# Optimization experiments

Hardware: AMD Instinct MI355X
Metric: run time of the kernel (lower is better)

## Reference

```python
import jax, jax.numpy as jnp
import numpy as np

PATCH = 24  # self.current_patch
STRIDE = PATCH // 2


def _conv(x, w, b):
    # NCHW conv, SAME padding, stride 1 (= Conv2d(k=3, padding=1))
    y = jax.lax.conv_general_dilated(x, w, (1, 1), 'SAME',
                                     dimension_numbers=('NCHW', 'OIHW', 'NCHW'))
    return y + b[None, :, None, None]


def setup_inputs() -> dict:
    key = jax.random.key(0)
    ks = jax.random.split(key, 9)
    b, c, h, w = 2, 64, 192, 192
    s = 0.05  # keep sigmoid/tanh unsaturated
    return {
        'source': jax.random.normal(ks[0], (b, c, h, w), jnp.float32),
        'target': jax.random.normal(ks[1], (b, c, h, w), jnp.float32),
        # deform_net params (128->512->256->1)
        'W1': jax.random.normal(ks[2], (512, 128, 3, 3), jnp.float32) * s,
        'b1': jnp.zeros((512,), jnp.float32),
        'W2': jax.random.normal(ks[3], (256, 512, 3, 3), jnp.float32) * s,
        'b2': jnp.zeros((256,), jnp.float32),
        'W3': jax.random.normal(ks[4], (1, 256, 3, 3), jnp.float32) * s,
        'b3': jnp.zeros((1,), jnp.float32),
        # reg_net params (128->512->64->1); original declared 256 in-ch (bug), fixed to 128
        'Wr1': jax.random.normal(ks[5], (512, 128, 3, 3), jnp.float32) * s,
        'br1': jnp.zeros((512,), jnp.float32),
        'Wr2': jax.random.normal(ks[6], (64, 512, 3, 3), jnp.float32) * s,
        'br2': jnp.zeros((64,), jnp.float32),
        'Wr3': jax.random.normal(ks[7], (1, 64, 3, 3), jnp.float32) * s,
        'br3': jnp.zeros((1,), jnp.float32),
    }


def _attention(src, tgt, W1, b1, W2, b2, W3, b3):
    b, c, h, w = src.shape
    p, st = PATCH, STRIDE
    nH = (h - p) // st + 1
    nW = (w - p) // st + 1
    # patch gather indices
    r_idx = jnp.arange(nH)[:, None] * st + jnp.arange(p)[None, :]  # [nH, p]
    c_idx = jnp.arange(nW)[:, None] * st + jnp.arange(p)[None, :]  # [nW, p]
    # [b, c, nH, nW, p, p]
    def gather(x):
        return x[:, :, r_idx[:, None, :, None], c_idx[None, :, None, :]]
    ps = gather(src)
    pt = gather(tgt)
    # -> [b*nH*nW, 2c, p, p]  (one big batched conv replaces the python loop)
    pair = jnp.concatenate([ps, pt], axis=1)            # [b, 2c, nH, nW, p, p]
    pair = pair.transpose(0, 2, 3, 1, 4, 5).reshape(b * nH * nW, 2 * c, p, p)
    x = jax.nn.relu(_conv(pair, W1, b1))
    x = jax.nn.relu(_conv(x, W2, b2))
    score = jax.nn.sigmoid(_conv(x, W3, b3))            # [b*nH*nW, 1, p, p]
    score = score.reshape(b, nH, nW, 1, p, p).transpose(0, 3, 1, 2, 4, 5)  # [b,1,nH,nW,p,p]
    # overlap-add scatter (duplicate indices accumulate)
    R = jnp.broadcast_to(r_idx[:, None, :, None], (nH, nW, p, p))
    C = jnp.broadcast_to(c_idx[None, :, None, :], (nH, nW, p, p))
    att = jnp.zeros((b, 1, h, w), src.dtype).at[:, :, R, C].add(score)
    cnt = jnp.zeros((b, 1, h, w), src.dtype).at[:, :, R, C].add(1.0)
    return att / jnp.maximum(cnt, 1.0)


def reference(source, target, W1, b1, W2, b2, W3, b3, Wr1, br1, Wr2, br2, Wr3, br3):
    attention_map = _attention(source, target, W1, b1, W2, b2, W3, b3)
    x = jnp.concatenate([source, target], axis=1)       # [b, 128, h, w]
    x = jax.nn.relu(_conv(x, Wr1, br1))
    x = jax.nn.relu(_conv(x, Wr2, br2))
    registered = jnp.tanh(_conv(x, Wr3, br3))           # [b, 1, h, w]
    return registered, attention_map
```

## Files before the change

kernel.cpp:

```cpp
#include <hip/hip_runtime.h>
#include <cmath>

typedef _Float16 half8  __attribute__((ext_vector_type(8)));
typedef _Float16 half4v __attribute__((ext_vector_type(4)));
typedef float    float4v __attribute__((ext_vector_type(4)));

template<int N> __device__ __forceinline__ void vwait() {
    asm volatile("s_waitcnt vmcnt(%0)" :: "n"(N) : "memory");
}

template<int MT, int NT, int MODE>
__global__ __launch_bounds__(256, 2)
void mfma_conv(const _Float16* __restrict__ in, const _Float16* __restrict__ Wg,
               const float* __restrict__ bias, _Float16* __restrict__ out,
               int CI, int CO, int RSin, int RSout, int NB, int NC, int p0)
{
    constexpr int CHUNKS_PH = 3 * MT * 64;
    constexpr int STAGE_N   = CHUNKS_PH / 256;
    constexpr int VF        = STAGE_N + 9;
    __shared__ __align__(16) _Float16 sW[3][CHUNKS_PH * 8];

    const int tid  = threadIdx.x;
    const int wave = tid >> 6;
    const int lane = tid & 63;
    const int ll   = lane & 15;
    const int quad = lane >> 4;

    const int NSUB = NC * (9 / NT);
    const int id   = blockIdx.x;
    const int xcd  = id & 7;
    const int slot = id >> 3;
    const int unit = (slot / NSUB) * 8 + xcd;
    const int rem  = slot % NSUB;
    const int pxb  = rem / NC;
    const int co_t = rem % NC;
    if (unit >= NB) return;
    const int co0 = co_t * (MT * 16);
    const int pbase = pxb * (NT * 64) + wave * (NT * 16);

    if (slot & 1) __builtin_amdgcn_s_sleep(32);

    size_t in_base, out_base;
    int TY = 0, TX = 0;
    int b_off[NT], edge[NT];
    if (MODE == 0) {
        int pat = p0 + unit;
        int bb = pat / 225, remp = pat % 225;
        int pi = remp / 15, pj = remp % 15;
        in_base  = (size_t)bb * RSin * RSin * CI;
        out_base = (size_t)unit * 676 * CO;
        #pragma unroll
        for (int nt = 0; nt < NT; ++nt) {
            int p = pbase + nt * 16 + ll;
            int py = p / 24, px = p % 24;
            b_off[nt] = ((pi * 12 + py) * RSin + (pj * 12 + px)) * CI;
            edge[nt] = (py == 0 ? 1 : 0) | (py == 23 ? 2 : 0)
                     | (px == 0 ? 4 : 0) | (px == 23 ? 8 : 0);
        }
    } else if (MODE == 1) {
        in_base  = (size_t)unit * 676 * CI;
        out_base = (size_t)unit * 676 * CO;
        #pragma unroll
        for (int nt = 0; nt < NT; ++nt) {
            int p = pbase + nt * 16 + ll;
            b_off[nt] = ((p / 24) * RSin + (p % 24)) * CI;
            edge[nt] = 0;
        }
    } else {
        int tile = unit & 63, b = unit >> 6;
        TY = (tile >> 3) * 24; TX = (tile & 7) * 24;
        in_base  = (size_t)b * RSin * RSin * CI;
        out_base = (size_t)b * RSout * RSout * CO;
        #pragma unroll
        for (int nt = 0; nt < NT; ++nt) {
            int p = pbase + nt * 16 + ll;
            b_off[nt] = ((TY + p / 24) * RSin + (TX + p % 24)) * CI;
            edge[nt] = 0;
        }
    }

    auto stage = [&](int bufI, int ci0, int dy) {
        #pragma unroll
        for (int k = 0; k < STAGE_N; ++k) {
            int c = tid + k * 256;
            int lane_s = c & 63;
            int mtt = c >> 6;
            int mt = mtt % MT, dxl = mtt / MT;
            const _Float16* src =
                &Wg[((size_t)(co0 + mt * 16 + (lane_s & 15)) * 9 + (dy * 3 + dxl)) * CI
                    + ci0 + (lane_s >> 4) * 8];
            __builtin_amdgcn_global_load_lds(
                (const __attribute__((address_space(1))) void*)src,
                (__attribute__((address_space(3))) void*)&sW[bufI][(size_t)c * 8],
                16, 0, 0);
        }
    };

    auto bload = [&](uint4 (&B)[NT][3], int ci0, int dy) {
        const _Float16* inp = in + in_base + ci0 + quad * 8;
        const int rowoff = dy * RSin * CI;
        #pragma unroll
        for (int nt = 0; nt < NT; ++nt)
            #pragma unroll
            for (int dx = 0; dx < 3; ++dx)
                B[nt][dx] = *(const uint4*)(inp + b_off[nt] + rowoff + dx * CI);
    };

    float4v acc[MT][NT];
    #pragma unroll
    for (int mt = 0; mt < MT; ++mt)
        #pragma unroll
        for (int nt = 0; nt < NT; ++nt)
            acc[mt][nt] = (float4v){0.f, 0.f, 0.f, 0.f};

    auto compute = [&](int bufI, uint4 (&B)[NT][3], int dy) {
        #pragma unroll
        for (int dx = 0; dx < 3; ++dx) {
            const int emask = (dy == 0 ? 1 : 0) | (dy == 2 ? 2 : 0)
                            | (dx == 0 ? 4 : 0) | (dx == 2 ? 8 : 0);
            half8 a[MT];
            #pragma unroll
            for (int mt = 0; mt < MT; ++mt)
                a[mt] = *(const half8*)&sW[bufI][((dx * MT + mt) * 64 + lane) * 8];
            #pragma unroll
            for (int nt = 0; nt < NT; ++nt) {
                uint4 raw = B[nt][dx];
                if (MODE == 0) {
                    bool z = (edge[nt] & emask) != 0;
                    raw.x = z ? 0u : raw.x;
                    raw.y = z ? 0u : raw.y;
                    raw.z = z ? 0u : raw.z;
                    raw.w = z ? 0u : raw.w;
                }
                half8 b = *(half8*)&raw;
                #pragma unroll
                for (int mt = 0; mt < MT; ++mt)
                    acc[mt][nt] = __builtin_amdgcn_mfma_f32_16x16x32_f16(
                        a[mt], b, acc[mt][nt], 0, 0, 0);
            }
        }
    };

    uint4 bA[NT][3], bB[NT][3];

    const int phases = (CI >> 5) * 3;
    stage(0, 0, 0);
    stage(1, 0, 1);
    bload(bA, 0, 0);

    int bufC = 0, dyC = 0, ciC = 0;
    int bufS = 2, dyS = 2, ciS = 0;
    int dyB = 1, ciB = 0;

#define ADV(dy, ci) do { if (dy == 2) { dy = 0; ci += 32; } else ++dy; } while (0)
#define PH(BCUR, BNXT, HASS, HASB, VN)                                      \
    do {                                                                    \
        __builtin_amdgcn_s_barrier();                                       \
        if (HASS) { stage(bufS, ciS, dyS);                                  \
                    bufS = (bufS == 2) ? 0 : bufS + 1; ADV(dyS, ciS); }     \
        if (HASB) { bload(BNXT, ciB, dyB); ADV(dyB, ciB); }                 \
        vwait<VN>();                                                        \
        __builtin_amdgcn_sched_barrier(0);                                  \
        __builtin_amdgcn_s_setprio(1);                                      \
        compute(bufC, BCUR, dyC);                                           \
        __builtin_amdgcn_s_setprio(0);                                      \
        bufC = (bufC == 2) ? 0 : bufC + 1; ADV(dyC, ciC);                   \
    } while (0)

    for (int it = 0; it < (phases - 6) / 2; ++it) {
        PH(bA, bB, 1, 1, VF);
        PH(bB, bA, 1, 1, VF);
    }
    PH(bA, bB, 1, 1, VF);
    PH(bB, bA, 1, 1, VF);
    PH(bA, bB, 1, 1, VF);
    PH(bB, bA, 1, 1, VF);
    PH(bA, bB, 0, 1, 9);
    PH(bB, bA, 0, 0, 0);
#undef PH
#undef ADV

    #pragma unroll
    for (int mt = 0; mt < MT; ++mt) {
        float4v bs = *(const float4v*)&bias[co0 + mt * 16 + quad * 4];
        #pragma unroll
        for (int nt = 0; nt < NT; ++nt) {
            int p = pbase + nt * 16 + ll;
            size_t ooff = out_base
                + (size_t)((TY + p / 24 + 1) * RSout + (TX + p % 24) + 1) * CO
                + co0 + mt * 16 + quad * 4;
            float4v v = acc[mt][nt];
            half4v h;
            h.x = (_Float16)fmaxf(v.x + bs.x, 0.f);
            h.y = (_Float16)fmaxf(v.y + bs.y, 0.f);
            h.z = (_Float16)fmaxf(v.z + bs.z, 0.f);
            h.w = (_Float16)fmaxf(v.w + bs.w, 0.f);
            *(half4v*)(out + ooff) = h;
        }
    }
}

static inline int swiz_grid(int NB, int NC, int PXB) {
    return ((NB + 7) & ~7) * NC * PXB;
}

template<int MODE, int ACT, int NT>
__global__ __launch_bounds__(256, 2)
void mfma_score(const _Float16* __restrict__ in, const _Float16* __restrict__ W16,
                const float* __restrict__ bias, float* __restrict__ outp,
                int CI, int RSI, int NB, int PXB)
{
    __shared__ __align__(16) _Float16 sW[9 * 16 * 32];

    const int tid  = threadIdx.x;
    const int wave = tid >> 6;
    const int lane = tid & 63;
    const int ll   = lane & 15;
    const int quad = lane >> 4;

    const int unit = blockIdx.x / PXB;
    const int pxb  = blockIdx.x % PXB;
    if (unit >= NB) return;
    const int pbase = pxb * (NT * 64) + wave * (NT * 16);

    size_t in_base;
    int ty = 0, tx = 0, bb = 0;
    if (MODE == 2) {
        bb = unit >> 6; int tile = unit & 63; ty = (tile >> 3) * 24; tx = (tile & 7) * 24;
        in_base = (size_t)bb * RSI * RSI * CI;
    } else {
        in_base = (size_t)unit * 676 * CI;
    }

    int b_off[NT];
    #pragma unroll
    for (int nt = 0; nt < NT; ++nt) {
        int p = pbase + nt * 16 + ll;
        b_off[nt] = ((ty + p / 24) * RSI + (tx + p % 24)) * CI;
    }

    float4v acc[NT];
    #pragma unroll
    for (int nt = 0; nt < NT; ++nt) acc[nt] = (float4v){0.f, 0.f, 0.f, 0.f};

    for (int ci0 = 0; ci0 < CI; ci0 += 32) {
        __syncthreads();
        for (int c = tid; c < 9 * 16 * 4; c += 256) {
            int q = c & 3, tco = c >> 2;
            int t = tco >> 4, co = tco & 15;
            *(uint4*)&sW[tco * 32 + q * 8] =
                *(const uint4*)&W16[((size_t)co * 9 + t) * CI + ci0 + q * 8];
        }
        __syncthreads();

        const _Float16* inp = in + in_base + ci0 + quad * 8;
        for (int dy = 0; dy < 3; ++dy)
            for (int dx = 0; dx < 3; ++dx) {
                const int t = dy * 3 + dx;
                const int toff = (dy * RSI + dx) * CI;
                half8 a = *(const half8*)&sW[(t * 16 + ll) * 32 + quad * 8];
                #pragma unroll
                for (int nt = 0; nt < NT; ++nt) {
                    half8 b = *(const half8*)(inp + b_off[nt] + toff);
                    acc[nt] = __builtin_amdgcn_mfma_f32_16x16x32_f16(a, b, acc[nt], 0, 0, 0);
                }
            }
    }

    if (quad == 0) {
        float bv = bias[0];
        #pragma unroll
        for (int nt = 0; nt < NT; ++nt) {
            int p = pbase + nt * 16 + ll;
            float v = acc[nt].x + bv;
            if (ACT == 1) {
                outp[(size_t)unit * 576 + p] = 1.f / (1.f + expf(-v));
            } else {
                int y = ty + p / 24, x = tx + p % 24;
                outp[(size_t)bb * 36864 + y * 192 + x] = tanhf(v);
            }
        }
    }
}

__global__ __launch_bounds__(256)
void build_x16i(const float* __restrict__ src, const float* __restrict__ tgt,
                _Float16* __restrict__ X)
{
    int idx = blockIdx.x * 256 + threadIdx.x;
    int q = idx & 15, pid = idx >> 4;
    if (pid >= 2 * 36864) return;
    int b = pid / 36864, r = pid % 36864;
    int y = r / 192, x = r % 192;
    half8 h;
    #pragma unroll
    for (int j = 0; j < 8; ++j) {
        int ch = q * 8 + j;
        const float* im = (ch < 64) ? src : tgt;
        h[j] = (_Float16)im[(size_t)(b * 64 + (ch & 63)) * 36864 + r];
    }
    *(half8*)&X[(((size_t)b * 194 + y + 1) * 194 + (x + 1)) * 128 + q * 8] = h;
}

__global__ __launch_bounds__(256)
void cvt_w(const float* __restrict__ src, _Float16* __restrict__ dst, int CO, int CI)
{
    int idx = blockIdx.x * 256 + threadIdx.x;
    if (idx >= CO * 9 * CI) return;
    int ci = idx % CI, t = (idx / CI) % 9, co = idx / (9 * CI);
    dst[idx] = (_Float16)src[((size_t)co * CI + ci) * 9 + t];
}

__global__ __launch_bounds__(256)
void cvt_pad16(const float* __restrict__ src, _Float16* __restrict__ dst, int CI)
{
    int idx = blockIdx.x * 256 + threadIdx.x;
    if (idx >= 16 * 9 * CI) return;
    int ci = idx % CI, t = (idx / CI) % 9, co = idx / (9 * CI);
    dst[idx] = (co == 0) ? (_Float16)src[(size_t)ci * 9 + t] : (_Float16)0.0f;
}

__global__ __launch_bounds__(256)
void ring_zero(_Float16* __restrict__ buf, int npatch, int RS, int CI)
{
    int c8 = CI >> 3;
    int RC = 2 * RS + 2 * (RS - 2);
    int idx = blockIdx.x * 256 + threadIdx.x;
    if (idx >= npatch * RC * c8) return;
    int q = idx % c8, rp = (idx / c8) % RC, pl = idx / (c8 * RC);
    int r, c;
    if (rp < RS)            { r = 0;      c = rp; }
    else if (rp < 2 * RS)   { r = RS - 1; c = rp - RS; }
    else {
        int s = rp - 2 * RS, half = RS - 2;
        if (s < half) { r = s + 1;        c = 0; }
        else          { r = s - half + 1; c = RS - 1; }
    }
    uint4 z = {0u, 0u, 0u, 0u};
    *(uint4*)&buf[((size_t)pl * RS * RS + r * RS + c) * CI + q * 8] = z;
}

__global__ __launch_bounds__(256)
void att_finalize(const float* __restrict__ score, float* __restrict__ out)
{
    int idx = blockIdx.x * 256 + threadIdx.x;
    if (idx >= 2 * 36864) return;
    int b = idx / 36864, r = idx % 36864;
    int y = r / 192, x = r % 192;
    int i_lo = (y >= 24) ? (y - 12) / 12 : 0;
    int i_hi = min(14, y / 12);
    int j_lo = (x >= 24) ? (x - 12) / 12 : 0;
    int j_hi = min(14, x / 12);
    float s = 0.f; int cnt = 0;
    for (int i = i_lo; i <= i_hi; ++i)
        for (int j = j_lo; j <= j_hi; ++j) {
            s += score[(((size_t)b * 15 + i) * 15 + j) * 576 + (y - 12 * i) * 24 + (x - 12 * j)];
            ++cnt;
        }
    out[idx] = s / (float)cnt;
}

extern "C" void kernel_launch(void* const* d_in, const int* in_sizes, int n_in,
                              void* d_out, int out_size, void* d_ws, size_t ws_size,
                              hipStream_t stream)
{
    const float* src = (const float*)d_in[0];
    const float* tgt = (const float*)d_in[1];
    const float* W1  = (const float*)d_in[2];  const float* b1  = (const float*)d_in[3];
    const float* W2  = (const float*)d_in[4];  const float* b2  = (const float*)d_in[5];
    const float* W3  = (const float*)d_in[6];  const float* b3  = (const float*)d_in[7];
    const float* Wr1 = (const float*)d_in[8];  const float* br1 = (const float*)d_in[9];
    const float* Wr2 = (const float*)d_in[10]; const float* br2 = (const float*)d_in[11];
    const float* Wr3 = (const float*)d_in[12]; const float* br3 = (const float*)d_in[13];
    float* out = (float*)d_out;

    _Float16* ws = (_Float16*)d_ws;
    size_t o = 0;
    _Float16* X16i = ws + o; o += (size_t)2 * 194 * 194 * 128;
    _Float16* W1h  = ws + o; o += (size_t)512 * 9 * 128;
    _Float16* W2h  = ws + o; o += (size_t)256 * 9 * 512;
    _Float16* Wr1h = ws + o; o += (size_t)512 * 9 * 128;
    _Float16* Wr2h = ws + o; o += (size_t)64 * 9 * 512;
    _Float16* W3p  = ws + o; o += (size_t)16 * 9 * 256;
    _Float16* Wr3p = ws + o; o += (size_t)16 * 9 * 64;
    float*    score = (float*)(ws + o); o += 2 * 259200;
    const size_t fixed_h = o;

    const size_t per_patch_h = (size_t)676 * (512 + 256);
    const size_t regA_h = (size_t)2 * 194 * 194 * 512;
    const size_t regB_h = (size_t)2 * 194 * 194 * 64;
    size_t h_avail = ws_size / 2;
    int P = 50;
    {
        size_t n450 = 450 * per_patch_h; if (n450 < regA_h + regB_h) n450 = regA_h + regB_h;
        size_t n150 = 150 * per_patch_h; if (n150 < regA_h + regB_h) n150 = regA_h + regB_h;
        if (h_avail >= fixed_h + n450)      P = 450;
        else if (h_avail >= fixed_h + n150) P = 150;
    }
    const int nchunks = 450 / P;

    _Float16* D1 = ws + fixed_h;
    _Float16* D2 = D1 + (size_t)P * 676 * 512;

    ring_zero<<<(2 * 772 * 16 + 255) / 256, 256, 0, stream>>>(X16i, 2, 194, 128);
    build_x16i<<<4608, 256, 0, stream>>>(src, tgt, X16i);
    cvt_w<<<2304, 256, 0, stream>>>(W1,  W1h,  512, 128);
    cvt_w<<<4608, 256, 0, stream>>>(W2,  W2h,  256, 512);
    cvt_w<<<2304, 256, 0, stream>>>(Wr1, Wr1h, 512, 128);
    cvt_w<<<1152, 256, 0, stream>>>(Wr2, Wr2h, 64,  512);
    cvt_pad16<<<(16 * 9 * 256 + 255) / 256, 256, 0, stream>>>(W3,  W3p,  256);
    cvt_pad16<<<(16 * 9 * 64  + 255) / 256, 256, 0, stream>>>(Wr3, Wr3p, 64);

    ring_zero<<<(P * 100 * 64 + 255) / 256, 256, 0, stream>>>(D1, P, 26, 512);
    ring_zero<<<(P * 100 * 32 + 255) / 256, 256, 0, stream>>>(D2, P, 26, 256);
    for (int c = 0; c < nchunks; ++c) {
        int p0 = c * P;
        mfma_conv<8, 3, 0><<<swiz_grid(P, 4, 3), 256, 0, stream>>>(
            X16i, W1h, b1, D1, 128, 512, 194, 26, P, 4, p0);
        mfma_conv<8, 3, 1><<<swiz_grid(P, 2, 3), 256, 0, stream>>>(
            D1, W2h, b2, D2, 512, 256, 26, 26, P, 2, 0);
        mfma_score<1, 1, 3><<<P * 3, 256, 0, stream>>>(
            D2, W3p, b3, score + (size_t)p0 * 576, 256, 26, P, 3);
    }
    att_finalize<<<288, 256, 0, stream>>>(score, out + 73728);

    {
        _Float16* A1 = ws + fixed_h;
        _Float16* A2 = A1 + ((P >= 150) ? regA_h : (size_t)194 * 194 * 512);
        if (P >= 150) {
            ring_zero<<<(2 * 772 * 64 + 255) / 256, 256, 0, stream>>>(A1, 2, 194, 512);
            ring_zero<<<(2 * 772 * 8  + 255) / 256, 256, 0, stream>>>(A2, 2, 194, 64);
            mfma_conv<8, 3, 2><<<swiz_grid(128, 4, 3), 256, 0, stream>>>(
                X16i, Wr1h, br1, A1, 128, 512, 194, 194, 128, 4, 0);
            mfma_conv<4, 3, 2><<<swiz_grid(128, 1, 3), 256, 0, stream>>>(
                A1, Wr2h, br2, A2, 512, 64, 194, 194, 128, 1, 0);
            mfma_score<2, 2, 3><<<128 * 3, 256, 0, stream>>>(
                A2, Wr3p, br3, out, 64, 194, 128, 3);
        } else {
            for (int b = 0; b < 2; ++b) {
                ring_zero<<<(772 * 64 + 255) / 256, 256, 0, stream>>>(A1, 1, 194, 512);
                ring_zero<<<(772 * 8  + 255) / 256, 256, 0, stream>>>(A2, 1, 194, 64);
                mfma_conv<8, 3, 2><<<swiz_grid(64, 4, 3), 256, 0, stream>>>(
                    X16i + (size_t)b * 194 * 194 * 128, Wr1h, br1, A1,
                    128, 512, 194, 194, 64, 4, 0);
                mfma_conv<4, 3, 2><<<swiz_grid(64, 1, 3), 256, 0, stream>>>(
                    A1, Wr2h, br2, A2, 512, 64, 194, 194, 64, 1, 0);
                mfma_score<2, 2, 3><<<64 * 3, 256, 0, stream>>>(
                    A2, Wr3p, br3, out + (size_t)b * 36864, 64, 194, 64, 3);
            }
        }
    }
}
```

Before: 2.231 ms.

## Flatten pixel tiling across patches and retile conv to MT=4, NT=4

```diff
diff --git a/kernel.cpp b/kernel.cpp
--- a/kernel.cpp
+++ b/kernel.cpp
@@ -17,7 +17,9 @@
 {
     constexpr int CHUNKS_PH = 3 * MT * 64;
     constexpr int STAGE_N   = CHUNKS_PH / 256;
-    constexpr int VF        = STAGE_N + 9;
+    constexpr int BLOAD_N   = 3 * NT;
+    constexpr int VF        = STAGE_N + BLOAD_N;
+    constexpr int PXBLK     = NT * 64;
     __shared__ __align__(16) _Float16 sW[3][CHUNKS_PH * 8];
 
     const int tid  = threadIdx.x;
@@ -26,55 +28,52 @@
     const int ll   = lane & 15;
     const int quad = lane >> 4;
 
-    const int NSUB = NC * (9 / NT);
+    const int Gpx  = (NB * 576 + PXBLK - 1) / PXBLK;
     const int id   = blockIdx.x;
     const int xcd  = id & 7;
     const int slot = id >> 3;
-    const int unit = (slot / NSUB) * 8 + xcd;
-    const int rem  = slot % NSUB;
-    const int pxb  = rem / NC;
-    const int co_t = rem % NC;
-    if (unit >= NB) return;
+    const int pxblk = (slot / NC) * 8 + xcd;
+    const int co_t  = slot % NC;
+    if (pxblk >= Gpx) return;
     const int co0 = co_t * (MT * 16);
-    const int pbase = pxb * (NT * 64) + wave * (NT * 16);
-
-    if (slot & 1) __builtin_amdgcn_s_sleep(32);
-
-    size_t in_base, out_base;
-    int TY = 0, TX = 0;
-    int b_off[NT], edge[NT];
-    if (MODE == 0) {
-        int pat = p0 + unit;
-        int bb = pat / 225, remp = pat % 225;
-        int pi = remp / 15, pj = remp % 15;
-        in_base  = (size_t)bb * RSin * RSin * CI;
-        out_base = (size_t)unit * 676 * CO;
-        #pragma unroll
-        for (int nt = 0; nt < NT; ++nt) {
-            int p = pbase + nt * 16 + ll;
-            int py = p / 24, px = p % 24;
-            b_off[nt] = ((pi * 12 + py) * RSin + (pj * 12 + px)) * CI;
+    const int pg0 = pxblk * PXBLK + wave * (NT * 16);
+
+    size_t b_off[NT], obase[NT];
+    int edge[NT];
+    bool valid[NT];
+    #pragma unroll
+    for (int nt = 0; nt < NT; ++nt) {
+        int pgn = pg0 + nt * 16 + ll;
+        int u = pgn / 576;
+        int p = pgn - u * 576;
+        valid[nt] = (u < NB);
+        int uu = valid[nt] ? u : 0;
+        int py = p / 24, px = p % 24;
+        if (MODE == 0) {
+            int pat = p0 + uu;
+            int bb = pat / 225, remp = pat % 225;
+            int pi = remp / 15, pj = remp % 15;
+            b_off[nt] = (size_t)bb * RSin * RSin * CI
+                      + (size_t)((pi * 12 + py) * RSin + (pj * 12 + px)) * CI
+                      + quad * 8;
+            obase[nt] = (size_t)uu * 676 * CO
+                      + (size_t)((py + 1) * RSout + (px + 1)) * CO;
             edge[nt] = (py == 0 ? 1 : 0) | (py == 23 ? 2 : 0)
                      | (px == 0 ? 4 : 0) | (px == 23 ? 8 : 0);
-        }
-    } else if (MODE == 1) {
-        in_base  = (size_t)unit * 676 * CI;
-        out_base = (size_t)unit * 676 * CO;
-        #pragma unroll
-        for (int nt = 0; nt < NT; ++nt) {
-            int p = pbase + nt * 16 + ll;
-            b_off[nt] = ((p / 24) * RSin + (p % 24)) * CI;
+        } else if (MODE == 1) {
+            b_off[nt] = (size_t)uu * 676 * CI + (size_t)(py * RSin + px) * CI
+                      + quad * 8;
+            obase[nt] = (size_t)uu * 676 * CO
+                      + (size_t)((py + 1) * RSout + (px + 1)) * CO;
             edge[nt] = 0;
-        }
-    } else {
-        int tile = unit & 63, b = unit >> 6;
-        TY = (tile >> 3) * 24; TX = (tile & 7) * 24;
-        in_base  = (size_t)b * RSin * RSin * CI;
-        out_base = (size_t)b * RSout * RSout * CO;
-        #pragma unroll
-        for (int nt = 0; nt < NT; ++nt) {
-            int p = pbase + nt * 16 + ll;
-            b_off[nt] = ((TY + p / 24) * RSin + (TX + p % 24)) * CI;
+        } else {
+            int bb = uu >> 6, tile = uu & 63;
+            int TY = (tile >> 3) * 24, TX = (tile & 7) * 24;
+            b_off[nt] = (size_t)bb * RSin * RSin * CI
+                      + (size_t)((TY + py) * RSin + (TX + px)) * CI
+                      + quad * 8;
+            obase[nt] = (size_t)bb * RSout * RSout * CO
+                      + (size_t)((TY + py + 1) * RSout + (TX + px + 1)) * CO;
             edge[nt] = 0;
         }
     }
@@ -97,13 +96,12 @@
     };
 
     auto bload = [&](uint4 (&B)[NT][3], int ci0, int dy) {
-        const _Float16* inp = in + in_base + ci0 + quad * 8;
-        const int rowoff = dy * RSin * CI;
+        const size_t rowoff = (size_t)(dy * RSin) * CI + ci0;
         #pragma unroll
         for (int nt = 0; nt < NT; ++nt)
             #pragma unroll
             for (int dx = 0; dx < 3; ++dx)
-                B[nt][dx] = *(const uint4*)(inp + b_off[nt] + rowoff + dx * CI);
+                B[nt][dx] = *(const uint4*)(in + b_off[nt] + rowoff + dx * CI);
     };
 
     float4v acc[MT][NT];
@@ -167,15 +165,11 @@
         bufC = (bufC == 2) ? 0 : bufC + 1; ADV(dyC, ciC);                   \
     } while (0)
 
-    for (int it = 0; it < (phases - 6) / 2; ++it) {
+    for (int it = 0; it < (phases - 2) / 2; ++it) {
         PH(bA, bB, 1, 1, VF);
         PH(bB, bA, 1, 1, VF);
     }
-    PH(bA, bB, 1, 1, VF);
-    PH(bB, bA, 1, 1, VF);
-    PH(bA, bB, 1, 1, VF);
-    PH(bB, bA, 1, 1, VF);
-    PH(bA, bB, 0, 1, 9);
+    PH(bA, bB, 0, 1, BLOAD_N);
     PH(bB, bA, 0, 0, 0);
 #undef PH
 #undef ADV
@@ -185,10 +179,8 @@
         float4v bs = *(const float4v*)&bias[co0 + mt * 16 + quad * 4];
         #pragma unroll
         for (int nt = 0; nt < NT; ++nt) {
-            int p = pbase + nt * 16 + ll;
-            size_t ooff = out_base
-                + (size_t)((TY + p / 24 + 1) * RSout + (TX + p % 24) + 1) * CO
-                + co0 + mt * 16 + quad * 4;
+            if (!valid[nt]) continue;
+            size_t ooff = obase[nt] + co0 + mt * 16 + quad * 4;
             float4v v = acc[mt][nt];
             half4v h;
             h.x = (_Float16)fmaxf(v.x + bs.x, 0.f);
@@ -200,8 +192,9 @@
     }
 }
 
-static inline int swiz_grid(int NB, int NC, int PXB) {
-    return ((NB + 7) & ~7) * NC * PXB;
+static inline int swiz_gridpx(int NB, int NT, int NC) {
+    int Gpx = (NB * 576 + NT * 64 - 1) / (NT * 64);
+    return ((Gpx + 7) & ~7) * NC;
 }
 
 template<int MODE, int ACT, int NT>
@@ -415,10 +408,10 @@
     ring_zero<<<(P * 100 * 32 + 255) / 256, 256, 0, stream>>>(D2, P, 26, 256);
     for (int c = 0; c < nchunks; ++c) {
         int p0 = c * P;
-        mfma_conv<8, 3, 0><<<swiz_grid(P, 4, 3), 256, 0, stream>>>(
-            X16i, W1h, b1, D1, 128, 512, 194, 26, P, 4, p0);
-        mfma_conv<8, 3, 1><<<swiz_grid(P, 2, 3), 256, 0, stream>>>(
-            D1, W2h, b2, D2, 512, 256, 26, 26, P, 2, 0);
+        mfma_conv<4, 4, 0><<<swiz_gridpx(P, 4, 8), 256, 0, stream>>>(
+            X16i, W1h, b1, D1, 128, 512, 194, 26, P, 8, p0);
+        mfma_conv<4, 4, 1><<<swiz_gridpx(P, 4, 4), 256, 0, stream>>>(
+            D1, W2h, b2, D2, 512, 256, 26, 26, P, 4, 0);
         mfma_score<1, 1, 3><<<P * 3, 256, 0, stream>>>(
             D2, W3p, b3, score + (size_t)p0 * 576, 256, 26, P, 3);
     }
@@ -430,9 +423,9 @@
         if (P >= 150) {
             ring_zero<<<(2 * 772 * 64 + 255) / 256, 256, 0, stream>>>(A1, 2, 194, 512);
             ring_zero<<<(2 * 772 * 8  + 255) / 256, 256, 0, stream>>>(A2, 2, 194, 64);
-            mfma_conv<8, 3, 2><<<swiz_grid(128, 4, 3), 256, 0, stream>>>(
-                X16i, Wr1h, br1, A1, 128, 512, 194, 194, 128, 4, 0);
-            mfma_conv<4, 3, 2><<<swiz_grid(128, 1, 3), 256, 0, stream>>>(
+            mfma_conv<4, 4, 2><<<swiz_gridpx(128, 4, 8), 256, 0, stream>>>(
+                X16i, Wr1h, br1, A1, 128, 512, 194, 194, 128, 8, 0);
+            mfma_conv<4, 4, 2><<<swiz_gridpx(128, 4, 1), 256, 0, stream>>>(
                 A1, Wr2h, br2, A2, 512, 64, 194, 194, 128, 1, 0);
             mfma_score<2, 2, 3><<<128 * 3, 256, 0, stream>>>(
                 A2, Wr3p, br3, out, 64, 194, 128, 3);
@@ -440,10 +433,10 @@
             for (int b = 0; b < 2; ++b) {
                 ring_zero<<<(772 * 64 + 255) / 256, 256, 0, stream>>>(A1, 1, 194, 512);
                 ring_zero<<<(772 * 8  + 255) / 256, 256, 0, stream>>>(A2, 1, 194, 64);
-                mfma_conv<8, 3, 2><<<swiz_grid(64, 4, 3), 256, 0, stream>>>(
+                mfma_conv<4, 4, 2><<<swiz_gridpx(64, 4, 8), 256, 0, stream>>>(
                     X16i + (size_t)b * 194 * 194 * 128, Wr1h, br1, A1,
-                    128, 512, 194, 194, 64, 4, 0);
-                mfma_conv<4, 3, 2><<<swiz_grid(64, 1, 3), 256, 0, stream>>>(
+                    128, 512, 194, 194, 64, 8, 0);
+                mfma_conv<4, 4, 2><<<swiz_gridpx(64, 4, 1), 256, 0, stream>>>(
                     A1, Wr2h, br2, A2, 512, 64, 194, 194, 64, 1, 0);
                 mfma_score<2, 2, 3><<<64 * 3, 256, 0, stream>>>(
                     A2, Wr3p, br3, out + (size_t)b * 36864, 64, 194, 64, 3);
```

Result: slower. 2.917 ms (+30.8%).
